# Optimization experiments

Hardware: AMD Instinct MI355X
Metric: run time of the kernel (lower is better)

The kernel has to match this reference:

```python
import jax, jax.numpy as jnp
import numpy as np
from jax import lax

HID = 128  # hidden_dim
K = 2      # kernel (must be 2 for the torch slice arithmetic to be shape-consistent)


def skew(x):
    # x: (B,C,H,W) -> (B,C,H,2W-1), row r shifted right by r
    B, C, H, W = x.shape
    rows = jnp.arange(H)[:, None]
    cols = jnp.arange(W)[None, :] + rows
    y = jnp.zeros((B, C, H, 2 * W - 1), x.dtype)
    return y.at[:, :, rows, cols].set(x)


def unskew(x):
    B, C, H, Wp = x.shape
    W = (Wp + 1) // 2
    rows = jnp.arange(H)[:, None]
    cols = jnp.arange(W)[None, :] + rows
    return x[:, :, rows, cols]


def setup_inputs() -> dict:
    key = jax.random.key(0)
    k1, k2, k3 = jax.random.split(key, 3)
    Cin = 128
    x = jax.random.normal(k1, (8, Cin, 64, 64), jnp.float32)
    w_is = jax.random.normal(k2, (4 * HID, Cin), jnp.float32) * 0.05   # 1x1 conv weight
    b_is = jnp.zeros((4 * HID,), jnp.float32)
    w_ss = jax.random.normal(k3, (4 * HID, HID, K, 1), jnp.float32) * 0.05  # (k,1) conv weight
    b_ss = jnp.zeros((4 * HID,), jnp.float32)
    return {"x": x, "w_is": w_is, "b_is": b_is, "w_ss": w_ss, "b_ss": b_ss}


def reference(x, w_is, b_is, w_ss, b_ss):
    B, Cin, H, W = x.shape
    hid, k = HID, K
    xs = skew(x)  # (B,Cin,H,2W-1)
    # input-to-state: 1x1 conv (mask B on 1x1 kernel == plain 1x1 conv)
    z_is = jnp.einsum('bchw,oc->bohw', xs, w_is) + b_is[None, :, None, None]
    steps = z_is.transpose(3, 0, 1, 2)  # (2W-1, B, 4hid, H)

    h0 = jnp.zeros((B, hid, H), x.dtype)
    c0 = jnp.zeros((B, hid, H), x.dtype)

    def step(carry, z_t):
        h, c = carry  # (B,hid,H)
        # state-to-state (k,1) conv along H, padding k//2, then drop last k-1 rows
        hs = lax.conv_general_dilated(h[..., None], w_ss, (1, 1),
                                      [(k // 2, k // 2), (0, 0)],
                                      dimension_numbers=('NCHW', 'OIHW', 'NCHW'))
        hs = hs[:, :, :-(k - 1), 0] + b_ss[None, :, None]  # (B,4hid,H)
        z = z_t + hs
        i = jax.nn.sigmoid(z[:, :hid])
        f = jax.nn.sigmoid(z[:, hid:2 * hid])
        o = jax.nn.sigmoid(z[:, 2 * hid:3 * hid])
        g = jnp.tanh(z[:, 3 * hid:])
        c = f * c + i * g
        h = o * jnp.tanh(c)
        return (h, c), h

    _, hs_all = lax.scan(step, (h0, c0), steps)  # (2W-1,B,hid,H)
    out = hs_all.transpose(1, 2, 3, 0)  # (B,hid,H,2W-1)
    return unskew(out)  # (B,hid,H,W)
```

## Files before the change

kernel.cpp:

```cpp
#include <hip/hip_runtime.h>
#include <hip/hip_fp16.h>
#include <math.h>


#define HID 128
#define BB 8
#define HH 64
#define WW 64
#define TT 127

#define NPREP 1022

typedef _Float16 v8h __attribute__((ext_vector_type(8)));
typedef float v4f __attribute__((ext_vector_type(4)));

#define SENT64 0xFFFFFFFFFFFFFFFFULL

__device__ __forceinline__ float fsig(float x) {
  float e = __builtin_amdgcn_exp2f(x * -1.44269504f);
  return __builtin_amdgcn_rcpf(1.f + e);
}
__device__ __forceinline__ float ftanh_(float x) {
  float e = __builtin_amdgcn_exp2f(x * 2.88539009f);
  return __builtin_fmaf(-2.f, __builtin_amdgcn_rcpf(1.f + e), 1.f);
}

__global__ __launch_bounds__(256) void prep_zpre(
    const float* __restrict__ x, const float* __restrict__ w_is,
    const float* __restrict__ b_is, const float* __restrict__ b_ss,
    const float* __restrict__ w_ss, _Float16* __restrict__ wp,
    __half* __restrict__ zph, unsigned long long* __restrict__ hx) {
  const int bid = blockIdx.x;
  const int tid = threadIdx.x;

  __shared__ _Float16 xt[64][136];

  if (bid < NPREP) {
    int idx = bid * 256 + tid;
    if (idx < 131072) {
      int j = idx & 7;
      int L = (idx >> 3) & 63;
      int kt = (idx >> 9) & 7;
      int mt = idx >> 12;
      int O = mt * 16 + (L & 15);
      int k = kt * 32 + ((L >> 4) & 3) * 8 + j;
      float v = (k < 128) ? w_ss[(size_t)O * 256 + k * 2]
                          : w_ss[(size_t)O * 256 + (k - 128) * 2 + 1];
      wp[idx] = (_Float16)v;
    } else if (idx < 131584) {
      int idx2 = idx - 131072;
      int g = (idx2 >> 2) & 3;
      int u = (idx2 >> 4) * 4 + (idx2 & 3);
      int O = g * 128 + u;
      zph[(size_t)BB * HH * WW * 512 + idx2] = __float2half(b_is[O] + b_ss[O]);
    } else {
      int j = idx - 131584;
      uint4 s;
      s.x = 0xFFFFFFFFu;
      s.y = 0xFFFFFFFFu;
      s.z = 0xFFFFFFFFu;
      s.w = 0xFFFFFFFFu;
      ((uint4*)hx)[j] = s;
    }
    return;
  }

  const int zb = bid - NPREP;
  const int b = zb >> 6;
  const int r = zb & 63;
  const int wv = tid >> 6;
  const int L = tid & 63;
  const int quad = L >> 4;
  const int l15 = L & 15;

  {
    const int cw = tid >> 4;
    const int w4 = (tid & 15) * 4;
#pragma unroll
    for (int p = 0; p < 8; p++) {
      int c = p * 16 + cw;
      float4 v = *(const float4*)&x[(((size_t)b * 128 + c) * HH + r) * WW + w4];
      xt[w4 + 0][c] = (_Float16)v.x;
      xt[w4 + 1][c] = (_Float16)v.y;
      xt[w4 + 2][c] = (_Float16)v.z;
      xt[w4 + 3][c] = (_Float16)v.w;
    }
  }

  v8h wfr[8][4];
  float4 bv[8];
#pragma unroll
  for (int m = 0; m < 8; m++) {
    const int mt = 8 * wv + m;
    const int O = mt * 16 + l15;
#pragma unroll
    for (int kt = 0; kt < 4; kt++) {
      const float* p = w_is + (size_t)O * 128 + kt * 32 + quad * 8;
      float4 a = *(const float4*)p;
      float4 b2 = *(const float4*)(p + 4);
      v8h f;
      f[0] = (_Float16)a.x;
      f[1] = (_Float16)a.y;
      f[2] = (_Float16)a.z;
      f[3] = (_Float16)a.w;
      f[4] = (_Float16)b2.x;
      f[5] = (_Float16)b2.y;
      f[6] = (_Float16)b2.z;
      f[7] = (_Float16)b2.w;
      wfr[m][kt] = f;
    }
    const int O4 = mt * 16 + quad * 4;
    float4 bi = *(const float4*)&b_is[O4];
    float4 bs4 = *(const float4*)&b_ss[O4];
    bv[m] = make_float4(bi.x + bs4.x, bi.y + bs4.y, bi.z + bs4.z, bi.w + bs4.w);
  }

  __syncthreads();

#pragma unroll
  for (int nt = 0; nt < 4; nt++) {
    v8h bf[4];
#pragma unroll
    for (int kt = 0; kt < 4; kt++)
      bf[kt] = *(const v8h*)&xt[nt * 16 + l15][kt * 32 + quad * 8];
    const size_t pos = ((size_t)b * HH + r) * WW + nt * 16 + l15;
#pragma unroll
    for (int m = 0; m < 8; m++) {
      v4f acc = (v4f){0.f, 0.f, 0.f, 0.f};
#pragma unroll
      for (int kt = 0; kt < 4; kt++)
        acc = __builtin_amdgcn_mfma_f32_16x16x32_f16(wfr[m][kt], bf[kt], acc,
                                                     0, 0, 0);
      const int mt = 8 * wv + m;
      __half2 lo = __floats2half2_rn(acc[0] + bv[m].x, acc[1] + bv[m].y);
      __half2 hi = __floats2half2_rn(acc[2] + bv[m].z, acc[3] + bv[m].w);
      uint2 pk;
      pk.x = *(unsigned*)&lo;
      pk.y = *(unsigned*)&hi;
      *(uint2*)&zph[pos * 512 + (m * 4 + quad) * 16 + wv * 4] = pk;
    }
  }
}

#define HROW 136

#define STEP_BARRIER()                                   \
  do {                                                   \
    asm volatile("s_waitcnt lgkmcnt(0)" ::: "memory");   \
    __builtin_amdgcn_s_barrier();                        \
    asm volatile("" ::: "memory");                       \
  } while (0)

#define STEP_BODY(T, RB)                                                       \
  do {                                                                         \
           \
    v8h bfr[4];                                                                \
    _Pragma("unroll") for (int kt = 0; kt < 4; kt++)                           \
        bfr[kt] = *(const v8h*)&h_lds[RB][(rl * 2 + bl) * HROW + kt * 32 +     \
                                          quad * 8];                           \
         \
    v4f zi[4];                                                                 \
    _Pragma("unroll") for (int g = 0; g < 4; g++)                              \
        _Pragma("unroll") for (int i = 0; i < 4; i++)                          \
        zi[g][i] = __half2float(zu.h[g * 4 + i]);                              \
         \
    {                                                                          \
      const uint4* p = (const uint4*)(((unsigned)wn < WW) ? zcur : zbias);     \
      zu.q[0] = p[0];                                                          \
      zu.q[1] = p[1];                                                          \
      wn++;                                                                    \
      zcur += 512;                                                             \
    }                                                                          \
          \
    v4f acc0[4], acc1[4];                                                      \
    _Pragma("unroll") for (int g = 0; g < 4; g++) {                            \
      acc0[g] = (v4f){0.f, 0.f, 0.f, 0.f};                                     \
      acc1[g] = zi[g];                                                         \
    }                                                                          \
    _Pragma("unroll") for (int kt = 0; kt < 4; kt++) {                         \
      _Pragma("unroll") for (int g = 0; g < 4; g++)                            \
          acc0[g] = __builtin_amdgcn_mfma_f32_16x16x32_f16(                    \
              wfrag[g][kt], bfr[kt], acc0[g], 0, 0, 0);                        \
    }                                                                          \
    _Pragma("unroll") for (int kt = 0; kt < 4; kt++) {                         \
      v8h bf1 = *(const v8h*)&h_lds[RB][((rl + 1) * 2 + bl) * HROW + kt * 32 + \
                                        quad * 8];                             \
      _Pragma("unroll") for (int g = 0; g < 4; g++)                            \
          acc1[g] = __builtin_amdgcn_mfma_f32_16x16x32_f16(                    \
              wfrag[g][4 + kt], bf1, acc1[g], 0, 0, 0);                        \
    }                                                                          \
          \
    unsigned long long pend = 0ull;                                            \
    if (is_cons)                                                               \
      pend = __hip_atomic_load(ca, __ATOMIC_RELAXED,                           \
                               __HIP_MEMORY_SCOPE_AGENT);                      \
                        \
    const int w = (T)-r;                                                       \
    const bool inband = ((unsigned)w < WW);                                    \
    float hv[4];                                                               \
    _Pragma("unroll") for (int rg2 = 0; rg2 < 4; rg2++) {                      \
      float z0 = acc0[0][rg2] + acc1[0][rg2];                                  \
      float z1 = acc0[1][rg2] + acc1[1][rg2];                                  \
      float z2 = acc0[2][rg2] + acc1[2][rg2];                                  \
      float z3 = acc0[3][rg2] + acc1[3][rg2];                                  \
      float iv = fsig(z0);                                                     \
      float fv = fsig(z1);                                                     \
      float ov = fsig(z2);                                                     \
      float gv = ftanh_(z3);                                                   \
      c[rg2] = fv * c[rg2] + iv * gv;                                          \
      hv[rg2] = ov * ftanh_(c[rg2]);                                           \
    }                                                                          \
                       \
    __half2 plo = __floats2half2_rn(hv[0], hv[1]);                             \
    __half2 phi = __floats2half2_rn(hv[2], hv[3]);                             \
    {                                                                          \
      uint2 pk;                                                                \
      pk.x = *(unsigned*)&plo;                                                 \
      pk.y = *(unsigned*)&phi;                                                 \
      *(uint2*)&h_lds[(RB) ^ 1][((rl + 1) * 2 + bl) * HROW + uq0] = pk;        \
    }                                                                          \
              \
    if (rgr < 7 && l15 >= 14) {                                                \
      unsigned long long pk =                                                  \
          ((unsigned long long)*(unsigned*)&phi << 32) | *(unsigned*)&plo;     \
      __hip_atomic_store(pa, pk, __ATOMIC_RELAXED, __HIP_MEMORY_SCOPE_AGENT);  \
    }                                                                          \
    pa += 2048;                                                                \
             \
    _Pragma("unroll") for (int rg2 = 0; rg2 < 4; rg2++) {                      \
      outb[rg2].x = outb[rg2].y;                                               \
      outb[rg2].y = outb[rg2].z;                                               \
      outb[rg2].z = outb[rg2].w;                                               \
      outb[rg2].w = hv[rg2];                                                   \
    }                                                                          \
    if (inband && (w & 3) == 3) {                                              \
      *(float4*)op0 = outb[0];                                                 \
      *(float4*)op1 = outb[1];                                                 \
      *(float4*)op2 = outb[2];                                                 \
      *(float4*)op3 = outb[3];                                                 \
      op0 += 4;                                                                \
      op1 += 4;                                                                \
      op2 += 4;                                                                \
      op3 += 4;                                                                \
    }                                                                          \
                   \
    if (is_cons) {                                                             \
      while (__ballot(pend == SENT64) != 0ull) {                               \
        __builtin_amdgcn_s_sleep(1);                                           \
        pend = __hip_atomic_load(ca, __ATOMIC_RELAXED,                         \
                                 __HIP_MEMORY_SCOPE_AGENT);                    \
      }                                                                        \
      *(unsigned long long*)&h_lds[(RB) ^ 1][(0 * 2 + ebl) * HROW + eu] =      \
          pend;                                                                \
    }                                                                          \
    ca += 2048;                                                                \
    STEP_BARRIER();                                                            \
  } while (0)

__global__ __launch_bounds__(512, 1) void lstm_mfma(
    const __half* __restrict__ zph, const _Float16* __restrict__ wp,
    unsigned long long* __restrict__ hx,
    float* __restrict__ out) {
  const int blk = blockIdx.x;
  const int rgr = blk >> 2;
  const int bg = blk & 3;
  const int R0 = rgr * 8;
  const int tid = threadIdx.x;
  const int wv = tid >> 6;
  const int L = tid & 63;
  const int quad = L >> 4;
  const int l15 = L & 15;
  const int rl = l15 >> 1;
  const int bl = l15 & 1;
  const int b = bg * 2 + bl;
  const int r = R0 + rl;
  const int uq0 = 16 * wv + quad * 4;
  const int zoff = (4 * wv + quad) * 16;

  __shared__ _Float16 h_lds[2][9 * 2 * HROW];
  for (int i = tid; i < (2 * 9 * 2 * HROW) / 2; i += 512)
    ((unsigned*)h_lds)[i] = 0u;

  v8h wfrag[4][8];
  {
    const v8h* wp8 = (const v8h*)wp;
#pragma unroll
    for (int g = 0; g < 4; g++)
#pragma unroll
      for (int kt = 0; kt < 8; kt++)
        wfrag[g][kt] = wp8[((size_t)((8 * g + wv) * 8 + kt)) * 64 + L];
  }

  float c[4] = {0.f, 0.f, 0.f, 0.f};
  float4 outb[4];
#pragma unroll
  for (int i = 0; i < 4; i++) outb[i] = make_float4(0.f, 0.f, 0.f, 0.f);

  const int ebl = L >> 5;
  const int eu = (L & 31) * 4;
  const int exp_idx = bl * 32 + 4 * wv + quad;

  const bool is_cons = (wv == 0) && (rgr > 0);

  const __half* zpp = zph + ((size_t)b * HH + r) * WW * 512 + zoff;
  const __half* zbias = zph + (size_t)BB * HH * WW * 512 + zoff;
  const unsigned long long* ca =
      hx + (((size_t)(rgr > 0 ? rgr - 1 : 0) * 4 + bg) * 64 + L);
  unsigned long long* pa = hx + (((size_t)rgr * 4 + bg) * 64 + exp_idx);
  float* op0 = out + (((size_t)b * HID + uq0 + 0) * HH + r) * WW;
  float* op1 = out + (((size_t)b * HID + uq0 + 1) * HH + r) * WW;
  float* op2 = out + (((size_t)b * HID + uq0 + 2) * HH + r) * WW;
  float* op3 = out + (((size_t)b * HID + uq0 + 3) * HH + r) * WW;

  union ZU {
    uint4 q[2];
    __half h[16];
  } zu;
  {
    const uint4* p0 = (const uint4*)((r == 0) ? zpp : zbias);
    zu.q[0] = p0[0];
    zu.q[1] = p0[1];
  }
  int wn = 1 - r;
  const __half* zcur = zpp + (ptrdiff_t)wn * 512;

  __syncthreads();

  for (int t = 0; t < TT - 1; t += 2) {
    STEP_BODY(t, 0);
    STEP_BODY(t + 1, 1);
  }
  STEP_BODY(TT - 1, 0);
}

__global__ __launch_bounds__(256) void transpose_x(const float* __restrict__ x,
                                                   float* __restrict__ xT) {
  int b = blockIdx.x >> 6;
  int r = blockIdx.x & 63;
  __shared__ float tile[32][65];
  for (int cc = 0; cc < 4; cc++) {
    int cl = threadIdx.x >> 6;
    int w = threadIdx.x & 63;
#pragma unroll
    for (int k = 0; k < 8; k++) {
      int c_loc = k * 4 + cl;
      int c = cc * 32 + c_loc;
      tile[c_loc][w] = x[(((size_t)b * 128 + c) * HH + r) * WW + w];
    }
    __syncthreads();
    int cs = threadIdx.x & 31;
    int wp = threadIdx.x >> 5;
#pragma unroll
    for (int k = 0; k < 8; k++) {
      int w2 = wp * 8 + k;
      xT[(((size_t)b * HH + r) * WW + w2) * 128 + cc * 32 + cs] = tile[cs][w2];
    }
    __syncthreads();
  }
}

__global__ __launch_bounds__(256) void step_kernel(
    const float* __restrict__ x, const float* __restrict__ xT, int use_xT,
    const float* __restrict__ w_is, const float* __restrict__ b_is,
    const float* __restrict__ w_ss, const float* __restrict__ b_ss,
    const float* __restrict__ h_prev, float* __restrict__ h_next,
    float* __restrict__ c_state, float* __restrict__ out, int t) {
  const int rg = blockIdx.x;
  const int q = blockIdx.y;
  const int r0 = rg * 2;
  const int tid = threadIdx.x;
  const int o_loc = tid & 63;
  const int k4 = tid >> 6;
  const int g_ = o_loc >> 4;
  const int u_ = o_loc & 15;
  const int O = g_ * 128 + q * 16 + u_;
  const int i0 = k4 * 32;

  __shared__ __align__(16) float h_in[3][BB][HID];
  __shared__ float zred[16][4][65];

  for (int idx = tid; idx < 3 * BB * HID; idx += 256) {
    int row_sel = idx >> 10;
    int rem = idx & 1023;
    int b = rem >> 7;
    int u = rem & 127;
    int rr = r0 - 1 + row_sel;
    h_in[row_sel][b][u] = (rr >= 0) ? h_prev[((size_t)b * HH + rr) * HID + u] : 0.0f;
  }

  float wr0[32], wr1[32], wz[32];
  {
    const float4* wss4 = (const float4*)(w_ss + ((size_t)O * 128 + i0) * 2);
#pragma unroll
    for (int j = 0; j < 16; j++) {
      float4 v = wss4[j];
      wr0[2 * j] = v.x;
      wr1[2 * j] = v.y;
      wr0[2 * j + 1] = v.z;
      wr1[2 * j + 1] = v.w;
    }
    const float4* wis4 = (const float4*)(w_is + (size_t)O * 128 + i0);
#pragma unroll
    for (int j = 0; j < 8; j++) {
      float4 v = wis4[j];
      wz[4 * j] = v.x;
      wz[4 * j + 1] = v.y;
      wz[4 * j + 2] = v.z;
      wz[4 * j + 3] = v.w;
    }
  }

  __syncthreads();

  float acc[2][BB];
#pragma unroll
// ... 22 lines not shown
    }
  }

#pragma unroll
  for (int rl = 0; rl < 2; rl++) {
    int rr = r0 + rl;
    int wcol = t - rr;
    if (wcol >= 0 && wcol < WW) {
      if (use_xT) {
        for (int b = 0; b < BB; b++) {
          const float4* xp =
              (const float4*)(xT + (((size_t)b * HH + rr) * WW + wcol) * 128 + i0);
#pragma unroll
          for (int j = 0; j < 8; j++) {
            float4 v = xp[j];
            acc[rl][b] += wz[4 * j] * v.x + wz[4 * j + 1] * v.y +
                          wz[4 * j + 2] * v.z + wz[4 * j + 3] * v.w;
          }
        }
      } else {
        for (int b = 0; b < BB; b++) {
          const float* xb = x + (((size_t)b * 128 + i0) * HH + rr) * WW + wcol;
#pragma unroll
          for (int j = 0; j < 32; j++) {
            acc[rl][b] += wz[j] * xb[(size_t)j * HH * WW];
          }
        }
      }
    }
  }

#pragma unroll
  for (int rl = 0; rl < 2; rl++)
#pragma unroll
    for (int b = 0; b < BB; b++) zred[rl * 8 + b][k4][o_loc] = acc[rl][b];
  __syncthreads();

  {
    int u = tid >> 4;
    int cell = tid & 15;
    int rl = cell >> 3;
    int b = cell & 7;
    int rr = r0 + rl;
    float z[4];
#pragma unroll
    for (int gg = 0; gg < 4; gg++) {
      int ol = gg * 16 + u;
      float s = zred[cell][0][ol] + zred[cell][1][ol] + zred[cell][2][ol] +
                zred[cell][3][ol];
      int Og = gg * 128 + q * 16 + u;
      z[gg] = s + b_is[Og] + b_ss[Og];
    }
    float iv = 1.0f / (1.0f + expf(-z[0]));
    float fv = 1.0f / (1.0f + expf(-z[1]));
    float ov = 1.0f / (1.0f + expf(-z[2]));
    float gv = tanhf(z[3]);
    int U = q * 16 + u;
    size_t sidx = ((size_t)b * HH + rr) * HID + U;
    float cv = c_state[sidx];
    float cn = fv * cv + iv * gv;
    c_state[sidx] = cn;
    float hn = ov * tanhf(cn);
    h_next[sidx] = hn;
    int wcol = t - rr;
    if (wcol >= 0 && wcol < WW) {
      out[(((size_t)b * HID + U) * HH + rr) * WW + wcol] = hn;
    }
  }
}

extern "C" void kernel_launch(void* const* d_in, const int* in_sizes, int n_in,
                              void* d_out, int out_size, void* d_ws,
                              size_t ws_size, hipStream_t stream) {
  const float* x = (const float*)d_in[0];
  const float* w_is = (const float*)d_in[1];
  const float* b_is = (const float*)d_in[2];
  const float* w_ss = (const float*)d_in[3];
  const float* b_ss = (const float*)d_in[4];
  float* outp = (float*)d_out;

  const size_t zph_bytes = ((size_t)BB * HH * WW * 512 + 512) * 2;
  const size_t wp_bytes = (size_t)512 * 256 * 2;
  const size_t hx_bytes = (size_t)TT * 8 * 4 * 64 * 8;
  const size_t need = zph_bytes + wp_bytes + hx_bytes;

  char* ws = (char*)d_ws;
  if (ws_size >= need) {
    __half* zph = (__half*)ws;
    _Float16* wpp = (_Float16*)(ws + zph_bytes);
    unsigned long long* hx =
        (unsigned long long*)(ws + zph_bytes + wp_bytes);

    prep_zpre<<<dim3(NPREP + 512), 256, 0, stream>>>(x, w_is, b_is, b_ss,
                                                     w_ss, wpp, zph, hx);
    lstm_mfma<<<dim3(32), 512, 0, stream>>>(zph, wpp, hx, outp);
  } else {
    const size_t xT_elems = (size_t)BB * HH * WW * 128;
    const size_t st_elems = (size_t)BB * HH * HID;
    const size_t need_xT = (xT_elems + 3 * st_elems) * sizeof(float);
    float* wsf = (float*)d_ws;
    float* xT = nullptr;
    float* st;
    int use_xT = 0;
    if (ws_size >= need_xT) {
      use_xT = 1;
      xT = wsf;
      st = wsf + xT_elems;
    } else {
      st = wsf;
    }
    float* h0 = st;
    float* h1 = st + st_elems;
    float* cb = st + 2 * st_elems;
    hipMemsetAsync(st, 0, 3 * st_elems * sizeof(float), stream);
    if (use_xT) transpose_x<<<dim3(BB * HH), 256, 0, stream>>>(x, xT);
    for (int t = 0; t < TT; t++) {
      float* hp = (t & 1) ? h1 : h0;
      float* hn = (t & 1) ? h0 : h1;
      step_kernel<<<dim3(32, 8), 256, 0, stream>>>(x, xT, use_xT, w_is, b_is,
                                                   w_ss, b_ss, hp, hn, cb, outp,
                                                   t);
    }
  }
}
```

Before: 290.9 us.

## Split LSTM hidden units across two blocks exchanging half-state via global memory

Adds a 64-block variant of the persistent LSTM kernel in which each block computes half of the hidden units (256 threads) and gets the other half of h from its partner block through per-step global buffers polled with sentinel values. The goal is to spread the serial recurrence over twice as many CUs, which shortens each step's MFMA and gate work. In exchange every step now needs a cross-block handshake through global memory with spin-waiting, and the prep kernel must also initialise the larger exchange buffer. The older 32-block path is kept as a fallback when the workspace is too small.

```diff
diff --git a/kernel.cpp b/kernel.cpp
--- a/kernel.cpp
+++ b/kernel.cpp
@@ -9,7 +9,11 @@
 #define WW 64
 #define TT 127
 
-#define NPREP 1022
+#define HROW 136
+#define HPSTEP (64 * 256)
+
+#define NPREP64 5118
+#define NPREP32 1022
 
 typedef _Float16 v8h __attribute__((ext_vector_type(8)));
 typedef float v4f __attribute__((ext_vector_type(4)));
@@ -29,13 +33,14 @@
     const float* __restrict__ x, const float* __restrict__ w_is,
     const float* __restrict__ b_is, const float* __restrict__ b_ss,
     const float* __restrict__ w_ss, _Float16* __restrict__ wp,
-    __half* __restrict__ zph, unsigned long long* __restrict__ hx) {
+    __half* __restrict__ zph, unsigned long long* __restrict__ hx,
+    unsigned long long* __restrict__ hp, int nprep) {
   const int bid = blockIdx.x;
   const int tid = threadIdx.x;
 
   __shared__ _Float16 xt[64][136];
 
-  if (bid < NPREP) {
+  if (bid < nprep) {
     int idx = bid * 256 + tid;
     if (idx < 131072) {
       int j = idx & 7;
@@ -53,19 +58,24 @@
       int u = (idx2 >> 4) * 4 + (idx2 & 3);
       int O = g * 128 + u;
       zph[(size_t)BB * HH * WW * 512 + idx2] = __float2half(b_is[O] + b_ss[O]);
-    } else {
+    } else if (idx < 261632) {
       int j = idx - 131584;
       uint4 s;
-      s.x = 0xFFFFFFFFu;
-      s.y = 0xFFFFFFFFu;
-      s.z = 0xFFFFFFFFu;
-      s.w = 0xFFFFFFFFu;
+      s.x = 0xFFFFFFFFu; s.y = 0xFFFFFFFFu;
+      s.z = 0xFFFFFFFFu; s.w = 0xFFFFFFFFu;
       ((uint4*)hx)[j] = s;
+    } else {
+      int j = idx - 261632;
+      uint4 s;
+      if (j < 8192) { s.x = 0u; s.y = 0u; s.z = 0u; s.w = 0u; }
+      else { s.x = 0xFFFFFFFFu; s.y = 0xFFFFFFFFu;
+             s.z = 0xFFFFFFFFu; s.w = 0xFFFFFFFFu; }
+      ((uint4*)hp)[j] = s;
     }
     return;
   }
 
-  const int zb = bid - NPREP;
+  const int zb = bid - nprep;
   const int b = zb >> 6;
   const int r = zb & 63;
   const int wv = tid >> 6;
@@ -99,14 +109,10 @@
       float4 a = *(const float4*)p;
       float4 b2 = *(const float4*)(p + 4);
       v8h f;
-      f[0] = (_Float16)a.x;
-      f[1] = (_Float16)a.y;
-      f[2] = (_Float16)a.z;
-      f[3] = (_Float16)a.w;
-      f[4] = (_Float16)b2.x;
-      f[5] = (_Float16)b2.y;
-      f[6] = (_Float16)b2.z;
-      f[7] = (_Float16)b2.w;
+      f[0] = (_Float16)a.x;  f[1] = (_Float16)a.y;
+      f[2] = (_Float16)a.z;  f[3] = (_Float16)a.w;
+      f[4] = (_Float16)b2.x; f[5] = (_Float16)b2.y;
+      f[6] = (_Float16)b2.z; f[7] = (_Float16)b2.w;
       wfr[m][kt] = f;
     }
     const int O4 = mt * 16 + quad * 4;
@@ -131,7 +137,6 @@
       for (int kt = 0; kt < 4; kt++)
         acc = __builtin_amdgcn_mfma_f32_16x16x32_f16(wfr[m][kt], bf[kt], acc,
                                                      0, 0, 0);
-      const int mt = 8 * wv + m;
       __half2 lo = __floats2half2_rn(acc[0] + bv[m].x, acc[1] + bv[m].y);
       __half2 hi = __floats2half2_rn(acc[2] + bv[m].z, acc[3] + bv[m].w);
       uint2 pk;
@@ -142,8 +147,6 @@
   }
 }
 
-#define HROW 136
-
 #define STEP_BARRIER()                                   \
   do {                                                   \
     asm volatile("s_waitcnt lgkmcnt(0)" ::: "memory");   \
@@ -151,19 +154,35 @@
     asm volatile("" ::: "memory");                       \
   } while (0)
 
-#define STEP_BODY(T, RB)                                                       \
+#define HPLD(p) __hip_atomic_load((p), __ATOMIC_RELAXED, __HIP_MEMORY_SCOPE_AGENT)
+
+#define STEP64(T, RB)                                                          \
   do {                                                                         \
-           \
-    v8h bfr[4];                                                                \
-    _Pragma("unroll") for (int kt = 0; kt < 4; kt++)                           \
-        bfr[kt] = *(const v8h*)&h_lds[RB][(rl * 2 + bl) * HROW + kt * 32 +     \
-                                          quad * 8];                           \
-         \
+                         \
+    v8h f0a = *(const v8h*)&h_lds[RB][(rl * 2 + bl) * HROW + oa * 32 +         \
+                                      quad * 8];                               \
+    v8h f0b = *(const v8h*)&h_lds[RB][(rl * 2 + bl) * HROW + (oa + 1) * 32 +   \
+                                      quad * 8];                               \
+    v8h f1a = *(const v8h*)&h_lds[RB][((rl + 1) * 2 + bl) * HROW + oa * 32 +   \
+                                      quad * 8];                               \
+    v8h f1b = *(const v8h*)&h_lds[RB][((rl + 1) * 2 + bl) * HROW +             \
+                                      (oa + 1) * 32 + quad * 8];               \
+                             \
+    unsigned long long P0a = HPLD(hpq + o0);                                   \
+    unsigned long long P0b = HPLD(hpq + o0 + 16);                              \
+    unsigned long long P0c = HPLD(hpq + o0 + 128);                             \
+    unsigned long long P0d = HPLD(hpq + o0 + 144);                             \
+    unsigned long long P1a = HPLD(hpq + o1);                                   \
+    unsigned long long P1b = HPLD(hpq + o1 + 16);                              \
+    unsigned long long P1c = HPLD(hpq + o1 + 128);                             \
+    unsigned long long P1d = HPLD(hpq + o1 + 144);                             \
+    if (!p0v) { P0a = 0ull; P0b = 0ull; P0c = 0ull; P0d = 0ull; }              \
+                               \
     v4f zi[4];                                                                 \
     _Pragma("unroll") for (int g = 0; g < 4; g++)                              \
         _Pragma("unroll") for (int i = 0; i < 4; i++)                          \
         zi[g][i] = __half2float(zu.h[g * 4 + i]);                              \
-         \
+                                                      \
     {                                                                          \
       const uint4* p = (const uint4*)(((unsigned)wn < WW) ? zcur : zbias);     \
       zu.q[0] = p[0];                                                          \
@@ -171,30 +190,69 @@
       wn++;                                                                    \
       zcur += 512;                                                             \
     }                                                                          \
-          \
+                                                          \
     v4f acc0[4], acc1[4];                                                      \
     _Pragma("unroll") for (int g = 0; g < 4; g++) {                            \
       acc0[g] = (v4f){0.f, 0.f, 0.f, 0.f};                                     \
       acc1[g] = zi[g];                                                         \
     }                                                                          \
-    _Pragma("unroll") for (int kt = 0; kt < 4; kt++) {                         \
+    _Pragma("unroll") for (int g = 0; g < 4; g++)                              \
+        acc0[g] = __builtin_amdgcn_mfma_f32_16x16x32_f16(wfrag[g][oa], f0a,    \
+                                                         acc0[g], 0, 0, 0);    \
+    _Pragma("unroll") for (int g = 0; g < 4; g++)                              \
+        acc0[g] = __builtin_amdgcn_mfma_f32_16x16x32_f16(wfrag[g][oa + 1],     \
+                                                         f0b, acc0[g], 0, 0,   \
+                                                         0);                   \
+    _Pragma("unroll") for (int g = 0; g < 4; g++)                              \
+        acc1[g] = __builtin_amdgcn_mfma_f32_16x16x32_f16(wfrag[g][4 + oa],     \
+                                                         f1a, acc1[g], 0, 0,   \
+                                                         0);                   \
+    _Pragma("unroll") for (int g = 0; g < 4; g++)                              \
+        acc1[g] = __builtin_amdgcn_mfma_f32_16x16x32_f16(wfrag[g][5 + oa],     \
+                                                         f1b, acc1[g], 0, 0,   \
+                                                         0);                   \
+                        \
+    while (__ballot(P0a == SENT64 || P0b == SENT64 || P0c == SENT64 ||         \
+                    P0d == SENT64 || P1a == SENT64 || P1b == SENT64 ||         \
+                    P1c == SENT64 || P1d == SENT64) != 0ull) {                 \
+      __builtin_amdgcn_s_sleep(1);                                             \
+      P0a = HPLD(hpq + o0);                                                    \
+      P0b = HPLD(hpq + o0 + 16);                                               \
+      P0c = HPLD(hpq + o0 + 128);                                              \
+      P0d = HPLD(hpq + o0 + 144);                                              \
+      P1a = HPLD(hpq + o1);                                                    \
+      P1b = HPLD(hpq + o1 + 16);                                               \
+      P1c = HPLD(hpq + o1 + 128);                                              \
+      P1d = HPLD(hpq + o1 + 144);                                              \
+      if (!p0v) { P0a = 0ull; P0b = 0ull; P0c = 0ull; P0d = 0ull; }            \
+    }                                                                          \
+                                                        \
+    {                                                                          \
+      union U2 { unsigned long long q[2]; v8h v; } uu;                         \
+      uu.q[0] = P0a; uu.q[1] = P0b; v8h g0a = uu.v;                            \
+      uu.q[0] = P0c; uu.q[1] = P0d; v8h g0b = uu.v;                            \
+      uu.q[0] = P1a; uu.q[1] = P1b; v8h g1a = uu.v;                            \
+      uu.q[0] = P1c; uu.q[1] = P1d; v8h g1b = uu.v;                            \
       _Pragma("unroll") for (int g = 0; g < 4; g++)                            \
-          acc0[g] = __builtin_amdgcn_mfma_f32_16x16x32_f16(                    \
-              wfrag[g][kt], bfr[kt], acc0[g], 0, 0, 0);                        \
-    }                                                                          \
-    _Pragma("unroll") for (int kt = 0; kt < 4; kt++) {                         \
-      v8h bf1 = *(const v8h*)&h_lds[RB][((rl + 1) * 2 + bl) * HROW + kt * 32 + \
-                                        quad * 8];                             \
+          acc0[g] = __builtin_amdgcn_mfma_f32_16x16x32_f16(wfrag[g][pa], g0a,  \
+                                                           acc0[g], 0, 0, 0);  \
       _Pragma("unroll") for (int g = 0; g < 4; g++)                            \
-          acc1[g] = __builtin_amdgcn_mfma_f32_16x16x32_f16(                    \
-              wfrag[g][4 + kt], bf1, acc1[g], 0, 0, 0);                        \
-    }                                                                          \
-          \
+          acc0[g] = __builtin_amdgcn_mfma_f32_16x16x32_f16(wfrag[g][pa + 1],   \
+                                                           g0b, acc0[g], 0, 0, \
+                                                           0);                 \
+      _Pragma("unroll") for (int g = 0; g < 4; g++)                            \
+          acc1[g] = __builtin_amdgcn_mfma_f32_16x16x32_f16(wfrag[g][4 + pa],   \
+                                                           g1a, acc1[g], 0, 0, \
+                                                           0);                 \
+      _Pragma("unroll") for (int g = 0; g < 4; g++)                            \
+          acc1[g] = __builtin_amdgcn_mfma_f32_16x16x32_f16(wfrag[g][5 + pa],   \
+                                                           g1b, acc1[g], 0, 0, \
+                                                           0);                 \
+    }                                                                          \
+                                     \
     unsigned long long pend = 0ull;                                            \
-    if (is_cons)                                                               \
-      pend = __hip_atomic_load(ca, __ATOMIC_RELAXED,                           \
-                               __HIP_MEMORY_SCOPE_AGENT);                      \
-                        \
+    if (cact) pend = HPLD(ca);                                                 \
+                                                                    \
     const int w = (T)-r;                                                       \
     const bool inband = ((unsigned)w < WW);                                    \
     float hv[4];                                                               \
@@ -210,7 +268,195 @@
       c[rg2] = fv * c[rg2] + iv * gv;                                          \
       hv[rg2] = ov * ftanh_(c[rg2]);                                           \
     }                                                                          \
-                       \
+                \
+    __half2 plo = __floats2half2_rn(hv[0], hv[1]);                             \
+    __half2 phi = __floats2half2_rn(hv[2], hv[3]);                             \
+    unsigned long long pk64 =                                                  \
+        ((unsigned long long)*(unsigned*)&phi << 32) | *(unsigned*)&plo;       \
+    {                                                                          \
+      uint2 pk;                                                                \
+      pk.x = *(unsigned*)&plo;                                                 \
+      pk.y = *(unsigned*)&phi;                                                 \
+      *(uint2*)&h_lds[(RB) ^ 1][((rl + 1) * 2 + bl) * HROW + uq0] = pk;        \
+    }                                                                          \
+    __hip_atomic_store(hpe, pk64, __ATOMIC_RELAXED, __HIP_MEMORY_SCOPE_AGENT); \
+    hpe += HPSTEP;                                                             \
+    if (rgr < 7 && l15 >= 14)                                                  \
+      __hip_atomic_store(pa_hx, pk64, __ATOMIC_RELAXED,                        \
+                         __HIP_MEMORY_SCOPE_AGENT);                            \
+    pa_hx += 2048;                                                             \
+                                                         \
+    _Pragma("unroll") for (int rg2 = 0; rg2 < 4; rg2++) {                      \
+      outb[rg2].x = outb[rg2].y;                                               \
+      outb[rg2].y = outb[rg2].z;                                               \
+      outb[rg2].z = outb[rg2].w;                                               \
+      outb[rg2].w = hv[rg2];                                                   \
+    }                                                                          \
+    if (inband && (w & 3) == 3) {                                              \
+      *(float4*)op0 = outb[0];                                                 \
+      *(float4*)op1 = outb[1];                                                 \
+      *(float4*)op2 = outb[2];                                                 \
+      *(float4*)op3 = outb[3];                                                 \
+      op0 += 4; op1 += 4; op2 += 4; op3 += 4;                                  \
+    }                                                                          \
+                                \
+    if (is_cons) {                                                             \
+      while (__ballot(cact && (pend == SENT64)) != 0ull) {                     \
+        __builtin_amdgcn_s_sleep(1);                                           \
+        if (cact) pend = HPLD(ca);                                             \
+      }                                                                        \
+      if (cact)                                                                \
+        *(unsigned long long*)&h_lds[(RB) ^ 1][(0 * 2 + ebl) * HROW + eu] =    \
+            pend;                                                              \
+    }                                                                          \
+    ca += 2048;                                                                \
+    hpq += HPSTEP;                                                             \
+    STEP_BARRIER();                                                            \
+  } while (0)
+
+__global__ __launch_bounds__(256, 1) void lstm_mfma64(
+    const __half* __restrict__ zph, const _Float16* __restrict__ wp,
+    unsigned long long* __restrict__ hx, unsigned long long* __restrict__ hp,
+    float* __restrict__ out) {
+  const int blk = blockIdx.x;
+  const int rgr = blk & 7;
+  const int mh = (blk >> 3) & 1;
+  const int bg = blk >> 4;
+  const int R0 = rgr * 8;
+  const int tid = threadIdx.x;
+  const int wv = tid >> 6;
+  const int L = tid & 63;
+  const int quad = L >> 4;
+  const int l15 = L & 15;
+  const int rl = l15 >> 1;
+  const int bl = l15 & 1;
+  const int b = bg * 2 + bl;
+  const int r = R0 + rl;
+  const int uq0 = mh * 64 + 16 * wv + quad * 4;
+  const int ug = uq0 >> 2;
+  const int zoff = ug * 16;
+  const int oa = 2 * mh;
+  const int pa = 2 * (1 - mh);
+
+  __shared__ _Float16 h_lds[2][9 * 2 * HROW];
+  for (int i = tid; i < (2 * 9 * 2 * HROW) / 2; i += 256)
+    ((unsigned*)h_lds)[i] = 0u;
+
+  v8h wfrag[4][8];
+  {
+    const v8h* wp8 = (const v8h*)wp;
+#pragma unroll
+    for (int g = 0; g < 4; g++)
+#pragma unroll
+      for (int kt = 0; kt < 8; kt++)
+        wfrag[g][kt] = wp8[((size_t)((8 * g + 4 * mh + wv) * 8 + kt)) * 64 + L];
+  }
+
+  float c[4] = {0.f, 0.f, 0.f, 0.f};
+  float4 outb[4];
+#pragma unroll
+  for (int i = 0; i < 4; i++) outb[i] = make_float4(0.f, 0.f, 0.f, 0.f);
+
+  const bool is_cons = (wv == 0) && (rgr > 0);
+  const bool cact = is_cons && (((L >> 4) & 1) == mh);
+  const int ebl = L >> 5;
+  const int eu = (L & 31) * 4;
+  const int exp_idx = bl * 32 + ug;
+  const unsigned long long* ca =
+      hx + (((size_t)(rgr > 0 ? rgr - 1 : 0) * 4 + bg)) * 64 + L;
+  unsigned long long* pa_hx = hx + (((size_t)rgr * 4 + bg)) * 64 + exp_idx;
+
+  const int pblk1 = blk ^ 8;
+  const int pblk0 = (rl > 0) ? pblk1 : ((rgr > 0) ? pblk1 - 1 : pblk1);
+  const bool p0v = (rl > 0) || (rgr > 0);
+  const int l15c0 = 2 * ((rl - 1) & 7) + bl;
+  const int l15c1 = 2 * rl + bl;
+  const int o0 = pblk0 * 256 + quad * 32 + l15c0;
+  const int o1 = pblk1 * 256 + quad * 32 + l15c1;
+  const unsigned long long* hpq = hp;
+  unsigned long long* hpe = hp + (size_t)HPSTEP + (size_t)blk * 256 + tid;
+
+  const __half* zpp = zph + ((size_t)b * HH + r) * WW * 512 + zoff;
+  const __half* zbias = zph + (size_t)BB * HH * WW * 512 + zoff;
+  float* op0 = out + (((size_t)b * HID + uq0 + 0) * HH + r) * WW;
+  float* op1 = out + (((size_t)b * HID + uq0 + 1) * HH + r) * WW;
+  float* op2 = out + (((size_t)b * HID + uq0 + 2) * HH + r) * WW;
+  float* op3 = out + (((size_t)b * HID + uq0 + 3) * HH + r) * WW;
+
+  union ZU {
+    uint4 q[2];
+    __half h[16];
+  } zu;
+  {
+    const uint4* p0 = (const uint4*)((r == 0) ? zpp : zbias);
+    zu.q[0] = p0[0];
+    zu.q[1] = p0[1];
+  }
+  int wn = 1 - r;
+  const __half* zcur = zpp + (ptrdiff_t)wn * 512;
+
+  __syncthreads();
+
+  for (int t = 0; t < TT - 1; t += 2) {
+    STEP64(t, 0);
+    STEP64(t + 1, 1);
+  }
+  STEP64(TT - 1, 0);
+}
+
+#define STEP_BODY(T, RB)                                                       \
+  do {                                                                         \
+    v8h bfr[4];                                                                \
+    _Pragma("unroll") for (int kt = 0; kt < 4; kt++)                           \
+        bfr[kt] = *(const v8h*)&h_lds[RB][(rl * 2 + bl) * HROW + kt * 32 +     \
+                                          quad * 8];                           \
+    v4f zi[4];                                                                 \
+    _Pragma("unroll") for (int g = 0; g < 4; g++)                              \
+        _Pragma("unroll") for (int i = 0; i < 4; i++)                          \
+        zi[g][i] = __half2float(zu.h[g * 4 + i]);                              \
+    {                                                                          \
+      const uint4* p = (const uint4*)(((unsigned)wn < WW) ? zcur : zbias);     \
+      zu.q[0] = p[0];                                                          \
+      zu.q[1] = p[1];                                                          \
+      wn++;                                                                    \
+      zcur += 512;                                                             \
+    }                                                                          \
+    v4f acc0[4], acc1[4];                                                      \
+    _Pragma("unroll") for (int g = 0; g < 4; g++) {                            \
+      acc0[g] = (v4f){0.f, 0.f, 0.f, 0.f};                                     \
+      acc1[g] = zi[g];                                                         \
+    }                                                                          \
+    _Pragma("unroll") for (int kt = 0; kt < 4; kt++) {                         \
+      _Pragma("unroll") for (int g = 0; g < 4; g++)                            \
+          acc0[g] = __builtin_amdgcn_mfma_f32_16x16x32_f16(                    \
+              wfrag[g][kt], bfr[kt], acc0[g], 0, 0, 0);                        \
+    }                                                                          \
+    _Pragma("unroll") for (int kt = 0; kt < 4; kt++) {                         \
+      v8h bf1 = *(const v8h*)&h_lds[RB][((rl + 1) * 2 + bl) * HROW + kt * 32 + \
+                                        quad * 8];                             \
+      _Pragma("unroll") for (int g = 0; g < 4; g++)                            \
+          acc1[g] = __builtin_amdgcn_mfma_f32_16x16x32_f16(                    \
+              wfrag[g][4 + kt], bf1, acc1[g], 0, 0, 0);                        \
+    }                                                                          \
+    unsigned long long pend = 0ull;                                            \
+    if (is_cons)                                                               \
+      pend = __hip_atomic_load(ca, __ATOMIC_RELAXED,                           \
+                               __HIP_MEMORY_SCOPE_AGENT);                      \
+    const int w = (T)-r;                                                       \
+    const bool inband = ((unsigned)w < WW);                                    \
+    float hv[4];                                                               \
+    _Pragma("unroll") for (int rg2 = 0; rg2 < 4; rg2++) {                      \
+      float z0 = acc0[0][rg2] + acc1[0][rg2];                                  \
+      float z1 = acc0[1][rg2] + acc1[1][rg2];                                  \
+      float z2 = acc0[2][rg2] + acc1[2][rg2];                                  \
+      float z3 = acc0[3][rg2] + acc1[3][rg2];                                  \
+      float iv = fsig(z0);                                                     \
+      float fv = fsig(z1);                                                     \
+      float ov = fsig(z2);                                                     \
+      float gv = ftanh_(z3);                                                   \
+      c[rg2] = fv * c[rg2] + iv * gv;                                          \
+      hv[rg2] = ov * ftanh_(c[rg2]);                                           \
+    }                                                                          \
     __half2 plo = __floats2half2_rn(hv[0], hv[1]);                             \
     __half2 phi = __floats2half2_rn(hv[2], hv[3]);                             \
     {                                                                          \
@@ -219,14 +465,12 @@
       pk.y = *(unsigned*)&phi;                                                 \
       *(uint2*)&h_lds[(RB) ^ 1][((rl + 1) * 2 + bl) * HROW + uq0] = pk;        \
     }                                                                          \
-              \
     if (rgr < 7 && l15 >= 14) {                                                \
       unsigned long long pk =                                                  \
           ((unsigned long long)*(unsigned*)&phi << 32) | *(unsigned*)&plo;     \
       __hip_atomic_store(pa, pk, __ATOMIC_RELAXED, __HIP_MEMORY_SCOPE_AGENT);  \
     }                                                                          \
     pa += 2048;                                                                \
-             \
     _Pragma("unroll") for (int rg2 = 0; rg2 < 4; rg2++) {                      \
       outb[rg2].x = outb[rg2].y;                                               \
       outb[rg2].y = outb[rg2].z;                                               \
@@ -238,12 +482,8 @@
       *(float4*)op1 = outb[1];                                                 \
       *(float4*)op2 = outb[2];                                                 \
       *(float4*)op3 = outb[3];                                                 \
-      op0 += 4;                                                                \
-      op1 += 4;                                                                \
-      op2 += 4;                                                                \
-      op3 += 4;                                                                \
-    }                                                                          \
-                   \
+      op0 += 4; op1 += 4; op2 += 4; op3 += 4;                                  \
+    }                                                                          \
     if (is_cons) {                                                             \
       while (__ballot(pend == SENT64) != 0ull) {                               \
         __builtin_amdgcn_s_sleep(1);                                           \
@@ -257,10 +497,9 @@
     STEP_BARRIER();                                                            \
   } while (0)
 
-__global__ __launch_bounds__(512, 1) void lstm_mfma(
+__global__ __launch_bounds__(512, 1) void lstm_mfma32(
     const __half* __restrict__ zph, const _Float16* __restrict__ wp,
-    unsigned long long* __restrict__ hx,
-    float* __restrict__ out) {
+    unsigned long long* __restrict__ hx, float* __restrict__ out) {
   const int blk = blockIdx.x;
   const int rgr = blk >> 2;
   const int bg = blk & 3;
@@ -519,18 +758,28 @@
   const size_t zph_bytes = ((size_t)BB * HH * WW * 512 + 512) * 2;
   const size_t wp_bytes = (size_t)512 * 256 * 2;
   const size_t hx_bytes = (size_t)TT * 8 * 4 * 64 * 8;
-  const size_t need = zph_bytes + wp_bytes + hx_bytes;
+  const size_t hp_bytes = (size_t)(TT + 1) * 64 * 256 * 8;
+  const size_t need32 = zph_bytes + wp_bytes + hx_bytes;
+  const size_t need64 = need32 + hp_bytes;
 
   char* ws = (char*)d_ws;
-  if (ws_size >= need) {
+  if (ws_size >= need64) {
     __half* zph = (__half*)ws;
     _Float16* wpp = (_Float16*)(ws + zph_bytes);
-    unsigned long long* hx =
-        (unsigned long long*)(ws + zph_bytes + wp_bytes);
-
-    prep_zpre<<<dim3(NPREP + 512), 256, 0, stream>>>(x, w_is, b_is, b_ss,
-                                                     w_ss, wpp, zph, hx);
-    lstm_mfma<<<dim3(32), 512, 0, stream>>>(zph, wpp, hx, outp);
+    unsigned long long* hx = (unsigned long long*)(ws + zph_bytes + wp_bytes);
+    unsigned long long* hp = (unsigned long long*)(ws + need32);
+
+    prep_zpre<<<dim3(NPREP64 + 512), 256, 0, stream>>>(
+        x, w_is, b_is, b_ss, w_ss, wpp, zph, hx, hp, NPREP64);
+    lstm_mfma64<<<dim3(64), 256, 0, stream>>>(zph, wpp, hx, hp, outp);
+  } else if (ws_size >= need32) {
+    __half* zph = (__half*)ws;
+    _Float16* wpp = (_Float16*)(ws + zph_bytes);
+    unsigned long long* hx = (unsigned long long*)(ws + zph_bytes + wp_bytes);
+
+    prep_zpre<<<dim3(NPREP32 + 512), 256, 0, stream>>>(
+        x, w_is, b_is, b_ss, w_ss, wpp, zph, hx, hx, NPREP32);
+    lstm_mfma32<<<dim3(32), 512, 0, stream>>>(zph, wpp, hx, outp);
   } else {
     const size_t xT_elems = (size_t)BB * HH * WW * 128;
     const size_t st_elems = (size_t)BB * HH * HID;
@@ -552,11 +801,11 @@
     hipMemsetAsync(st, 0, 3 * st_elems * sizeof(float), stream);
     if (use_xT) transpose_x<<<dim3(BB * HH), 256, 0, stream>>>(x, xT);
     for (int t = 0; t < TT; t++) {
-      float* hp = (t & 1) ? h1 : h0;
+      float* hp2 = (t & 1) ? h1 : h0;
       float* hn = (t & 1) ? h0 : h1;
       step_kernel<<<dim3(32, 8), 256, 0, stream>>>(x, xT, use_xT, w_is, b_is,
-                                                   w_ss, b_ss, hp, hn, cb, outp,
-                                                   t);
+                                                   w_ss, b_ss, hp2, hn, cb,
+                                                   outp, t);
     }
   }
 }
```

Result: slower. 762.6 us (+162.2%).

## Halve LSTM recurrence block to four waves, each computing two unit groups

Applied to the files above, without the earlier changes.

The recurrent LSTM kernel now runs with 256 threads (4 waves) per block instead of 512. Each wave holds two sets of weight fragments (A and B) and computes two groups of hidden units per step, doubling its MFMA, activation and output work. The goal is cheaper per-step barriers and more independent MFMA chains per wave, which helps hide latency. The cost is twice the register pressure from weight fragments, and each step's serial work per wave roughly doubles.

```diff
diff --git a/kernel.cpp b/kernel.cpp
--- a/kernel.cpp
+++ b/kernel.cpp
@@ -10,6 +10,8 @@
 #define TT 127
 
 #define NPREP 1022
+
+#define HROW 136
 
 typedef _Float16 v8h __attribute__((ext_vector_type(8)));
 typedef float v4f __attribute__((ext_vector_type(4)));
@@ -56,10 +58,8 @@
     } else {
       int j = idx - 131584;
       uint4 s;
-      s.x = 0xFFFFFFFFu;
-      s.y = 0xFFFFFFFFu;
-      s.z = 0xFFFFFFFFu;
-      s.w = 0xFFFFFFFFu;
+      s.x = 0xFFFFFFFFu; s.y = 0xFFFFFFFFu;
+      s.z = 0xFFFFFFFFu; s.w = 0xFFFFFFFFu;
       ((uint4*)hx)[j] = s;
     }
     return;
@@ -99,14 +99,10 @@
       float4 a = *(const float4*)p;
       float4 b2 = *(const float4*)(p + 4);
       v8h f;
-      f[0] = (_Float16)a.x;
-      f[1] = (_Float16)a.y;
-      f[2] = (_Float16)a.z;
-      f[3] = (_Float16)a.w;
-      f[4] = (_Float16)b2.x;
-      f[5] = (_Float16)b2.y;
-      f[6] = (_Float16)b2.z;
-      f[7] = (_Float16)b2.w;
+      f[0] = (_Float16)a.x;  f[1] = (_Float16)a.y;
+      f[2] = (_Float16)a.z;  f[3] = (_Float16)a.w;
+      f[4] = (_Float16)b2.x; f[5] = (_Float16)b2.y;
+      f[6] = (_Float16)b2.z; f[7] = (_Float16)b2.w;
       wfr[m][kt] = f;
     }
     const int O4 = mt * 16 + quad * 4;
@@ -131,7 +127,6 @@
       for (int kt = 0; kt < 4; kt++)
         acc = __builtin_amdgcn_mfma_f32_16x16x32_f16(wfr[m][kt], bf[kt], acc,
                                                      0, 0, 0);
-      const int mt = 8 * wv + m;
       __half2 lo = __floats2half2_rn(acc[0] + bv[m].x, acc[1] + bv[m].y);
       __half2 hi = __floats2half2_rn(acc[2] + bv[m].z, acc[3] + bv[m].w);
       uint2 pk;
@@ -142,8 +137,6 @@
   }
 }
 
-#define HROW 136
-
 #define STEP_BARRIER()                                   \
   do {                                                   \
     asm volatile("s_waitcnt lgkmcnt(0)" ::: "memory");   \
@@ -151,104 +144,146 @@
     asm volatile("" ::: "memory");                       \
   } while (0)
 
-#define STEP_BODY(T, RB)                                                       \
+#define HPLD(p) __hip_atomic_load((p), __ATOMIC_RELAXED, __HIP_MEMORY_SCOPE_AGENT)
+
+#define STEP4W(T, RB)                                                          \
   do {                                                                         \
-           \
-    v8h bfr[4];                                                                \
+         \
+    v8h bfr[4], bf1[4];                                                        \
     _Pragma("unroll") for (int kt = 0; kt < 4; kt++)                           \
         bfr[kt] = *(const v8h*)&h_lds[RB][(rl * 2 + bl) * HROW + kt * 32 +     \
                                           quad * 8];                           \
-         \
-    v4f zi[4];                                                                 \
+    _Pragma("unroll") for (int kt = 0; kt < 4; kt++)                           \
+        bf1[kt] = *(const v8h*)&h_lds[RB][((rl + 1) * 2 + bl) * HROW +         \
+                                          kt * 32 + quad * 8];                 \
+                        \
+    v4f ziA[4], ziB[4];                                                        \
     _Pragma("unroll") for (int g = 0; g < 4; g++)                              \
-        _Pragma("unroll") for (int i = 0; i < 4; i++)                          \
-        zi[g][i] = __half2float(zu.h[g * 4 + i]);                              \
-         \
+        _Pragma("unroll") for (int i = 0; i < 4; i++) {                        \
+      ziA[g][i] = __half2float(zuA.h[g * 4 + i]);                              \
+      ziB[g][i] = __half2float(zuB.h[g * 4 + i]);                              \
+    }                                                                          \
+               \
     {                                                                          \
       const uint4* p = (const uint4*)(((unsigned)wn < WW) ? zcur : zbias);     \
-      zu.q[0] = p[0];                                                          \
-      zu.q[1] = p[1];                                                          \
+      zuA.q[0] = p[0];                                                         \
+      zuA.q[1] = p[1];                                                         \
+      zuB.q[0] = p[32];                                                        \
+      zuB.q[1] = p[33];                                                        \
       wn++;                                                                    \
       zcur += 512;                                                             \
     }                                                                          \
-          \
-    v4f acc0[4], acc1[4];                                                      \
+                                 \
+    v4f a0[4], a1[4], b0[4], b1[4];                                            \
     _Pragma("unroll") for (int g = 0; g < 4; g++) {                            \
-      acc0[g] = (v4f){0.f, 0.f, 0.f, 0.f};                                     \
-      acc1[g] = zi[g];                                                         \
+      a0[g] = (v4f){0.f, 0.f, 0.f, 0.f};                                       \
+      b0[g] = (v4f){0.f, 0.f, 0.f, 0.f};                                       \
+      a1[g] = ziA[g];                                                          \
+      b1[g] = ziB[g];                                                          \
     }                                                                          \
     _Pragma("unroll") for (int kt = 0; kt < 4; kt++) {                         \
       _Pragma("unroll") for (int g = 0; g < 4; g++)                            \
-          acc0[g] = __builtin_amdgcn_mfma_f32_16x16x32_f16(                    \
-              wfrag[g][kt], bfr[kt], acc0[g], 0, 0, 0);                        \
+          a0[g] = __builtin_amdgcn_mfma_f32_16x16x32_f16(wfA[g][kt], bfr[kt],  \
+                                                         a0[g], 0, 0, 0);      \
+      _Pragma("unroll") for (int g = 0; g < 4; g++)                            \
+          b0[g] = __builtin_amdgcn_mfma_f32_16x16x32_f16(wfB[g][kt], bfr[kt],  \
+                                                         b0[g], 0, 0, 0);      \
     }                                                                          \
     _Pragma("unroll") for (int kt = 0; kt < 4; kt++) {                         \
-      v8h bf1 = *(const v8h*)&h_lds[RB][((rl + 1) * 2 + bl) * HROW + kt * 32 + \
-                                        quad * 8];                             \
       _Pragma("unroll") for (int g = 0; g < 4; g++)                            \
-          acc1[g] = __builtin_amdgcn_mfma_f32_16x16x32_f16(                    \
-              wfrag[g][4 + kt], bf1, acc1[g], 0, 0, 0);                        \
-    }                                                                          \
-          \
+          a1[g] = __builtin_amdgcn_mfma_f32_16x16x32_f16(wfA[g][4 + kt],       \
+                                                         bf1[kt], a1[g], 0, 0, \
+                                                         0);                   \
+      _Pragma("unroll") for (int g = 0; g < 4; g++)                            \
+          b1[g] = __builtin_amdgcn_mfma_f32_16x16x32_f16(wfB[g][4 + kt],       \
+                                                         bf1[kt], b1[g], 0, 0, \
+                                                         0);                   \
+    }                                                                          \
+                                     \
     unsigned long long pend = 0ull;                                            \
-    if (is_cons)                                                               \
-      pend = __hip_atomic_load(ca, __ATOMIC_RELAXED,                           \
-                               __HIP_MEMORY_SCOPE_AGENT);                      \
-                        \
+    if (is_cons) pend = HPLD(ca);                                              \
+                                                        \
     const int w = (T)-r;                                                       \
     const bool inband = ((unsigned)w < WW);                                    \
-    float hv[4];                                                               \
+    float hvA[4], hvB[4];                                                      \
     _Pragma("unroll") for (int rg2 = 0; rg2 < 4; rg2++) {                      \
-      float z0 = acc0[0][rg2] + acc1[0][rg2];                                  \
-      float z1 = acc0[1][rg2] + acc1[1][rg2];                                  \
-      float z2 = acc0[2][rg2] + acc1[2][rg2];                                  \
-      float z3 = acc0[3][rg2] + acc1[3][rg2];                                  \
+      float z0 = a0[0][rg2] + a1[0][rg2];                                      \
+      float z1 = a0[1][rg2] + a1[1][rg2];                                      \
+      float z2 = a0[2][rg2] + a1[2][rg2];                                      \
+      float z3 = a0[3][rg2] + a1[3][rg2];                                      \
       float iv = fsig(z0);                                                     \
       float fv = fsig(z1);                                                     \
       float ov = fsig(z2);                                                     \
       float gv = ftanh_(z3);                                                   \
-      c[rg2] = fv * c[rg2] + iv * gv;                                          \
-      hv[rg2] = ov * ftanh_(c[rg2]);                                           \
-    }                                                                          \
-                       \
-    __half2 plo = __floats2half2_rn(hv[0], hv[1]);                             \
-    __half2 phi = __floats2half2_rn(hv[2], hv[3]);                             \
+      cA[rg2] = fv * cA[rg2] + iv * gv;                                        \
+      hvA[rg2] = ov * ftanh_(cA[rg2]);                                         \
+    }                                                                          \
+    _Pragma("unroll") for (int rg2 = 0; rg2 < 4; rg2++) {                      \
+      float z0 = b0[0][rg2] + b1[0][rg2];                                      \
+      float z1 = b0[1][rg2] + b1[1][rg2];                                      \
+      float z2 = b0[2][rg2] + b1[2][rg2];                                      \
+      float z3 = b0[3][rg2] + b1[3][rg2];                                      \
+      float iv = fsig(z0);                                                     \
+      float fv = fsig(z1);                                                     \
+      float ov = fsig(z2);                                                     \
+      float gv = ftanh_(z3);                                                   \
+      cB[rg2] = fv * cB[rg2] + iv * gv;                                        \
+      hvB[rg2] = ov * ftanh_(cB[rg2]);                                         \
+    }                                                                          \
+                                            \
+    __half2 ploA = __floats2half2_rn(hvA[0], hvA[1]);                          \
+    __half2 phiA = __floats2half2_rn(hvA[2], hvA[3]);                          \
+    __half2 ploB = __floats2half2_rn(hvB[0], hvB[1]);                          \
+    __half2 phiB = __floats2half2_rn(hvB[2], hvB[3]);                          \
     {                                                                          \
       uint2 pk;                                                                \
-      pk.x = *(unsigned*)&plo;                                                 \
-      pk.y = *(unsigned*)&phi;                                                 \
+      pk.x = *(unsigned*)&ploA;                                                \
+      pk.y = *(unsigned*)&phiA;                                                \
       *(uint2*)&h_lds[(RB) ^ 1][((rl + 1) * 2 + bl) * HROW + uq0] = pk;        \
-    }                                                                          \
-              \
+      pk.x = *(unsigned*)&ploB;                                                \
+      pk.y = *(unsigned*)&phiB;                                                \
+      *(uint2*)&h_lds[(RB) ^ 1][((rl + 1) * 2 + bl) * HROW + uq0 + 64] = pk;   \
+    }                                                                          \
+            \
     if (rgr < 7 && l15 >= 14) {                                                \
-      unsigned long long pk =                                                  \
-          ((unsigned long long)*(unsigned*)&phi << 32) | *(unsigned*)&plo;     \
-      __hip_atomic_store(pa, pk, __ATOMIC_RELAXED, __HIP_MEMORY_SCOPE_AGENT);  \
-    }                                                                          \
-    pa += 2048;                                                                \
-             \
+      unsigned long long pkA =                                                 \
+          ((unsigned long long)*(unsigned*)&phiA << 32) | *(unsigned*)&ploA;   \
+      unsigned long long pkB =                                                 \
+          ((unsigned long long)*(unsigned*)&phiB << 32) | *(unsigned*)&ploB;   \
+      __hip_atomic_store(pa_hx, pkA, __ATOMIC_RELAXED,                         \
+                         __HIP_MEMORY_SCOPE_AGENT);                            \
+      __hip_atomic_store(pa_hx + 16, pkB, __ATOMIC_RELAXED,                    \
+                         __HIP_MEMORY_SCOPE_AGENT);                            \
+    }                                                                          \
+    pa_hx += 2048;                                                             \
+           \
     _Pragma("unroll") for (int rg2 = 0; rg2 < 4; rg2++) {                      \
-      outb[rg2].x = outb[rg2].y;                                               \
-      outb[rg2].y = outb[rg2].z;                                               \
-      outb[rg2].z = outb[rg2].w;                                               \
-      outb[rg2].w = hv[rg2];                                                   \
+      outbA[rg2].x = outbA[rg2].y;                                             \
+      outbA[rg2].y = outbA[rg2].z;                                             \
+      outbA[rg2].z = outbA[rg2].w;                                             \
+      outbA[rg2].w = hvA[rg2];                                                 \
+      outbB[rg2].x = outbB[rg2].y;                                             \
+      outbB[rg2].y = outbB[rg2].z;                                             \
+      outbB[rg2].z = outbB[rg2].w;                                             \
+      outbB[rg2].w = hvB[rg2];                                                 \
     }                                                                          \
     if (inband && (w & 3) == 3) {                                              \
-      *(float4*)op0 = outb[0];                                                 \
-      *(float4*)op1 = outb[1];                                                 \
-      *(float4*)op2 = outb[2];                                                 \
-      *(float4*)op3 = outb[3];                                                 \
-      op0 += 4;                                                                \
-      op1 += 4;                                                                \
-      op2 += 4;                                                                \
-      op3 += 4;                                                                \
-    }                                                                          \
-                   \
+      *(float4*)opA0 = outbA[0];                                               \
+      *(float4*)opA1 = outbA[1];                                               \
+      *(float4*)opA2 = outbA[2];                                               \
+      *(float4*)opA3 = outbA[3];                                               \
+      *(float4*)opB0 = outbB[0];                                               \
+      *(float4*)opB1 = outbB[1];                                               \
+      *(float4*)opB2 = outbB[2];                                               \
+      *(float4*)opB3 = outbB[3];                                               \
+      opA0 += 4; opA1 += 4; opA2 += 4; opA3 += 4;                              \
+      opB0 += 4; opB1 += 4; opB2 += 4; opB3 += 4;                              \
+    }                                                                          \
+                          \
     if (is_cons) {                                                             \
       while (__ballot(pend == SENT64) != 0ull) {                               \
         __builtin_amdgcn_s_sleep(1);                                           \
-        pend = __hip_atomic_load(ca, __ATOMIC_RELAXED,                         \
-                                 __HIP_MEMORY_SCOPE_AGENT);                    \
+        pend = HPLD(ca);                                                       \
       }                                                                        \
       *(unsigned long long*)&h_lds[(RB) ^ 1][(0 * 2 + ebl) * HROW + eu] =      \
           pend;                                                                \
@@ -257,7 +292,7 @@
     STEP_BARRIER();                                                            \
   } while (0)
 
-__global__ __launch_bounds__(512, 1) void lstm_mfma(
+__global__ __launch_bounds__(256, 1) void lstm_mfma4w(
     const __half* __restrict__ zph, const _Float16* __restrict__ wp,
     unsigned long long* __restrict__ hx,
     float* __restrict__ out) {
@@ -275,51 +310,64 @@
   const int b = bg * 2 + bl;
   const int r = R0 + rl;
   const int uq0 = 16 * wv + quad * 4;
-  const int zoff = (4 * wv + quad) * 16;
+  const int ugA = 4 * wv + quad;
+  const int zoffA = ugA * 16;
 
   __shared__ _Float16 h_lds[2][9 * 2 * HROW];
-  for (int i = tid; i < (2 * 9 * 2 * HROW) / 2; i += 512)
+  for (int i = tid; i < (2 * 9 * 2 * HROW) / 2; i += 256)
     ((unsigned*)h_lds)[i] = 0u;
 
-  v8h wfrag[4][8];
+  v8h wfA[4][8], wfB[4][8];
   {
     const v8h* wp8 = (const v8h*)wp;
 #pragma unroll
     for (int g = 0; g < 4; g++)
 #pragma unroll
-      for (int kt = 0; kt < 8; kt++)
-        wfrag[g][kt] = wp8[((size_t)((8 * g + wv) * 8 + kt)) * 64 + L];
-  }
-
-  float c[4] = {0.f, 0.f, 0.f, 0.f};
-  float4 outb[4];
-#pragma unroll
-  for (int i = 0; i < 4; i++) outb[i] = make_float4(0.f, 0.f, 0.f, 0.f);
+      for (int kt = 0; kt < 8; kt++) {
+        wfA[g][kt] = wp8[((size_t)((8 * g + wv) * 8 + kt)) * 64 + L];
+        wfB[g][kt] = wp8[((size_t)((8 * g + wv + 4) * 8 + kt)) * 64 + L];
+      }
+  }
+
+  float cA[4] = {0.f, 0.f, 0.f, 0.f};
+  float cB[4] = {0.f, 0.f, 0.f, 0.f};
+  float4 outbA[4], outbB[4];
+#pragma unroll
+  for (int i = 0; i < 4; i++) {
+    outbA[i] = make_float4(0.f, 0.f, 0.f, 0.f);
+    outbB[i] = make_float4(0.f, 0.f, 0.f, 0.f);
+  }
 
   const int ebl = L >> 5;
   const int eu = (L & 31) * 4;
-  const int exp_idx = bl * 32 + 4 * wv + quad;
+  const int exp_idx = bl * 32 + ugA;
 
   const bool is_cons = (wv == 0) && (rgr > 0);
 
-  const __half* zpp = zph + ((size_t)b * HH + r) * WW * 512 + zoff;
-  const __half* zbias = zph + (size_t)BB * HH * WW * 512 + zoff;
+  const __half* zpp = zph + ((size_t)b * HH + r) * WW * 512 + zoffA;
+  const __half* zbias = zph + (size_t)BB * HH * WW * 512 + zoffA;
   const unsigned long long* ca =
       hx + (((size_t)(rgr > 0 ? rgr - 1 : 0) * 4 + bg) * 64 + L);
-  unsigned long long* pa = hx + (((size_t)rgr * 4 + bg) * 64 + exp_idx);
-  float* op0 = out + (((size_t)b * HID + uq0 + 0) * HH + r) * WW;
-  float* op1 = out + (((size_t)b * HID + uq0 + 1) * HH + r) * WW;
-  float* op2 = out + (((size_t)b * HID + uq0 + 2) * HH + r) * WW;
-  float* op3 = out + (((size_t)b * HID + uq0 + 3) * HH + r) * WW;
+  unsigned long long* pa_hx = hx + (((size_t)rgr * 4 + bg) * 64 + exp_idx);
+  float* opA0 = out + (((size_t)b * HID + uq0 + 0) * HH + r) * WW;
+  float* opA1 = out + (((size_t)b * HID + uq0 + 1) * HH + r) * WW;
+  float* opA2 = out + (((size_t)b * HID + uq0 + 2) * HH + r) * WW;
+  float* opA3 = out + (((size_t)b * HID + uq0 + 3) * HH + r) * WW;
+  float* opB0 = out + (((size_t)b * HID + uq0 + 64) * HH + r) * WW;
+  float* opB1 = out + (((size_t)b * HID + uq0 + 65) * HH + r) * WW;
+  float* opB2 = out + (((size_t)b * HID + uq0 + 66) * HH + r) * WW;
+  float* opB3 = out + (((size_t)b * HID + uq0 + 67) * HH + r) * WW;
 
   union ZU {
     uint4 q[2];
     __half h[16];
-  } zu;
+  } zuA, zuB;
   {
     const uint4* p0 = (const uint4*)((r == 0) ? zpp : zbias);
-    zu.q[0] = p0[0];
-    zu.q[1] = p0[1];
+    zuA.q[0] = p0[0];
+    zuA.q[1] = p0[1];
+    zuB.q[0] = p0[32];
+    zuB.q[1] = p0[33];
   }
   int wn = 1 - r;
   const __half* zcur = zpp + (ptrdiff_t)wn * 512;
@@ -327,10 +375,10 @@
   __syncthreads();
 
   for (int t = 0; t < TT - 1; t += 2) {
-    STEP_BODY(t, 0);
-    STEP_BODY(t + 1, 1);
-  }
-  STEP_BODY(TT - 1, 0);
+    STEP4W(t, 0);
+    STEP4W(t + 1, 1);
+  }
+  STEP4W(TT - 1, 0);
 }
 
 __global__ __launch_bounds__(256) void transpose_x(const float* __restrict__ x,
@@ -530,7 +578,7 @@
 
     prep_zpre<<<dim3(NPREP + 512), 256, 0, stream>>>(x, w_is, b_is, b_ss,
                                                      w_ss, wpp, zph, hx);
-    lstm_mfma<<<dim3(32), 512, 0, stream>>>(zph, wpp, hx, outp);
+    lstm_mfma4w<<<dim3(32), 256, 0, stream>>>(zph, wpp, hx, outp);
   } else {
     const size_t xT_elems = (size_t)BB * HH * WW * 128;
     const size_t st_elems = (size_t)BB * HH * HID;
```

After: 435.4 us. 49.7% more time.
